# Kernel tuning notes

Measured on AMD Instinct MI355X. Metric: run time of the kernel, lower is better.

Reference implementation:

```python
import jax, jax.numpy as jnp
import numpy as np


def _conv2d(x, w, b, padding):
    # x: [N,C,H,W], w: [O,I,kh,kw]
    y = jax.lax.conv_general_dilated(
        x, w, window_strides=(1, 1), padding=padding,
        dimension_numbers=("NCHW", "OIHW", "NCHW"))
    return y + b[None, :, None, None]


def setup_inputs() -> dict:
    key = jax.random.key(0)
    ks = jax.random.split(key, 9)
    s = 0.05
    return {
        "x": jax.random.normal(ks[0], (16, 4, 512, 512), dtype=jnp.float32),
        "w1": jax.random.normal(ks[1], (32, 4, 3, 3), dtype=jnp.float32) * s,
        "b1": jax.random.normal(ks[2], (32,), dtype=jnp.float32) * s,
        "w2": jax.random.normal(ks[3], (4, 32, 3, 3), dtype=jnp.float32) * s,
        "b2": jax.random.normal(ks[4], (4,), dtype=jnp.float32) * s,
        "w_se1": jax.random.normal(ks[5], (16, 32, 1, 1), dtype=jnp.float32) * s,
        "b_se1": jax.random.normal(ks[6], (16,), dtype=jnp.float32) * s,
        "w_se2": jax.random.normal(ks[7], (32, 16, 1, 1), dtype=jnp.float32) * s,
        "b_se2": jax.random.normal(ks[8], (32,), dtype=jnp.float32) * s,
    }


def reference(x, w1, b1, w2, b2, w_se1, b_se1, w_se2, b_se2):
    x1 = x
    # module1: 3x3 conv (4->32) + ReLU
    h = jax.nn.relu(_conv2d(x, w1, b1, padding="SAME"))  # [N,32,H,W]
    se_in = h
    # SE branch: global avg pool -> 1x1 conv -> ReLU -> 1x1 conv -> sigmoid
    p = jnp.mean(h, axis=(2, 3), keepdims=True)  # [N,32,1,1]
    p = jax.nn.relu(_conv2d(p, w_se1, b_se1, padding="VALID"))  # [N,16,1,1]
    p = jax.nn.sigmoid(_conv2d(p, w_se2, b_se2, padding="VALID"))  # [N,32,1,1]
    h = p * se_in  # broadcast channel scaling
    # module2: 3x3 conv (32->4) + ReLU
    h = jax.nn.relu(_conv2d(h, w2, b2, padding="SAME"))  # [N,4,H,W]
    return h * x1  # residual multiply
```

## Files before the change

kernel.cpp:

```cpp
#include <hip/hip_runtime.h>
#include <math.h>

#define IMG 512

typedef __attribute__((ext_vector_type(4))) short short4_t;
typedef __attribute__((ext_vector_type(8))) short short8;
typedef __attribute__((ext_vector_type(4))) float f32x4;
typedef __attribute__((ext_vector_type(16))) float f32x16;
typedef __attribute__((ext_vector_type(2))) unsigned int u32x2;

__device__ __forceinline__ unsigned short f2bf(float f) {
  unsigned u = __builtin_bit_cast(unsigned, f);
  u += 0x7FFFu + ((u >> 16) & 1u);
  return (unsigned short)(u >> 16);
}
__device__ __forceinline__ unsigned cvtpk(float lo, float hi) {
  unsigned r;
  asm("v_cvt_pk_bf16_f32 %0, %1, %2" : "=v"(r) : "v"(lo), "v"(hi));
  return r;
}

__global__ __launch_bounds__(256) void k_prep(const float* __restrict__ w1,
                                              unsigned short* __restrict__ w1f) {
  const int t = threadIdx.x;
  if (t < 192) {
    const int kk = t >> 6, lane = t & 63;
    const int oc = lane & 31, hi = lane >> 5;
#pragma unroll
    for (int j = 0; j < 8; ++j) {
      const int dxp = 2 * hi + (j >> 2), ic = j & 3;
      float v = (dxp < 3) ? w1[((oc * 4 + ic) * 3 + kk) * 3 + dxp] : 0.f;
      w1f[(kk * 64 + lane) * 8 + j] = f2bf(v);
    }
  }
}

__global__ __launch_bounds__(256, 3) void k_pool(
    const float* __restrict__ x, const unsigned short* __restrict__ w1f,
    const float* __restrict__ b1, float* __restrict__ red_out, int use_atomic) {
  __shared__ unsigned short xs[34 * 40 * 4];
  __shared__ float pools[4][2][16];
  const int bid = blockIdx.x;
  const int swz = (bid & 7) * 512 + (bid >> 3);
  const int bx = swz & 15, by = (swz >> 4) & 15, n = swz >> 8;
  const int x0 = bx * 32, y0 = by * 32;
  const int t = threadIdx.x, lane = t & 63, wv = t >> 6;
  const int hi = lane >> 5;

  short8 A1[3];
#pragma unroll
  for (int kk = 0; kk < 3; ++kk)
    A1[kk] = *(const short8*)&w1f[(kk * 64 + lane) * 8];
  float bias_r[16];
#pragma unroll
  for (int r = 0; r < 16; ++r) {
    float bl = b1[(r & 3) + 8 * (r >> 2)], bh = b1[(r & 3) + 8 * (r >> 2) + 4];
    bias_r[r] = hi ? bh : bl;
  }

  const int sx = x0 - 4;
  const long CS = (long)IMG * IMG;
  for (int i = t; i < 340; i += 256) {
    const int row = i / 10, cb = i % 10;
    const int gy = y0 - 1 + row, gx0 = sx + cb * 4;
    f32x4 v0 = {0.f, 0.f, 0.f, 0.f}, v1 = v0, v2 = v0, v3 = v0;
    if (gy >= 0 && gy < IMG && gx0 >= 0 && gx0 < IMG) {
      const float* p = x + (((long)(n * 4) * IMG + gy) * IMG + gx0);
      v0 = *(const f32x4*)p;
      v1 = *(const f32x4*)(p + CS);
      v2 = *(const f32x4*)(p + 2 * CS);
      v3 = *(const f32x4*)(p + 3 * CS);
    }
    unsigned short* d = &xs[(row * 40 + cb * 4) * 4];
#pragma unroll
    for (int j = 0; j < 4; ++j) {
      u32x2 w;
      w[0] = cvtpk(v0[j], v1[j]);
      w[1] = cvtpk(v2[j], v3[j]);
      *(u32x2*)(d + j * 4) = w;
    }
  }
  __syncthreads();

  float pacc[16];
#pragma unroll
  for (int r = 0; r < 16; ++r) pacc[r] = 0.f;
  const int cx0 = (lane & 31) + 2 * hi + 3;
  const unsigned short* pP = &xs[((wv * 8) * 40 + cx0) * 4];
#define LOADP(K)                                                              \
  __builtin_shufflevector(*(const short4_t*)(pP + (K)*160),                   \
                          *(const short4_t*)(pP + (K)*160 + 4), 0, 1, 2, 3,   \
                          4, 5, 6, 7)
  short8 Ba, Bb, Bc;
  Ba = LOADP(0);
  Bb = LOADP(1);
#define P_ITER(IT, B0, B1, B2)                                                \
  {                                                                           \
    B2 = LOADP((IT) + 2);                                                     \
    f32x16 C;                                                                 \
    _Pragma("unroll") for (int r = 0; r < 16; ++r) C[r] = bias_r[r];          \
    C = __builtin_amdgcn_mfma_f32_32x32x16_bf16(A1[0], B0, C, 0, 0, 0);       \
    C = __builtin_amdgcn_mfma_f32_32x32x16_bf16(A1[1], B1, C, 0, 0, 0);       \
    C = __builtin_amdgcn_mfma_f32_32x32x16_bf16(A1[2], B2, C, 0, 0, 0);       \
    _Pragma("unroll") for (int r = 0; r < 16; ++r)                            \
        pacc[r] += fmaxf(C[r], 0.f);                                          \
  }
  P_ITER(0, Ba, Bb, Bc)
  P_ITER(1, Bb, Bc, Ba)
  P_ITER(2, Bc, Ba, Bb)
  P_ITER(3, Ba, Bb, Bc)
  P_ITER(4, Bb, Bc, Ba)
  P_ITER(5, Bc, Ba, Bb)
  P_ITER(6, Ba, Bb, Bc)
  P_ITER(7, Bb, Bc, Ba)
#undef P_ITER
#undef LOADP
#pragma unroll
  for (int r = 0; r < 16; ++r) {
#pragma unroll
    for (int m = 1; m < 32; m <<= 1) pacc[r] += __shfl_xor(pacc[r], m);
  }
  if ((lane & 31) == 0) {
#pragma unroll
    for (int r = 0; r < 16; ++r) pools[wv][hi][r] = pacc[r];
  }
  __syncthreads();
  if (t < 32) {
    const int c = t;
    const int hic = (c >> 2) & 1, reg = (c & 3) + 4 * (c >> 3);
    float s = pools[0][hic][reg] + pools[1][hic][reg] + pools[2][hic][reg] +
              pools[3][hic][reg];
    if (use_atomic) {
      atomicAdd(&red_out[n * 32 + c], s);
    } else {
      red_out[(n * 256 + by * 16 + bx) * 32 + c] = s;
    }
  }
}

__global__ __launch_bounds__(256) void k_se(
    const float* __restrict__ partials, const float* __restrict__ sums,
    const float* __restrict__ w_se1, const float* __restrict__ b_se1,
    const float* __restrict__ w_se2, const float* __restrict__ b_se2,
    const float* __restrict__ w2, unsigned short* __restrict__ w2f, int det) {
  const int n = blockIdx.x, t = threadIdx.x;
  __shared__ float red[8][32];
  __shared__ float mean_s[32], f1[16], p[32];
  if (det) {
    const int c = t & 31, s = t >> 5;
    float a = 0.f;
    for (int i = s * 32; i < s * 32 + 32; ++i)
      a += partials[(n * 256 + i) * 32 + c];
    red[s][c] = a;
    __syncthreads();
    if (t < 32) {
      float v = 0.f;
#pragma unroll
      for (int s2 = 0; s2 < 8; ++s2) v += red[s2][t];
      mean_s[t] = v * (1.0f / (512.f * 512.f));
    }
  } else {
    if (t < 32) mean_s[t] = sums[n * 32 + t] * (1.0f / (512.f * 512.f));
  }
  __syncthreads();
  if (t < 16) {
    float a = b_se1[t];
#pragma unroll
    for (int c = 0; c < 32; ++c) a += w_se1[t * 32 + c] * mean_s[c];
    f1[t] = fmaxf(a, 0.f);
  }
  __syncthreads();
  if (t < 32) {
    float a = b_se2[t];
#pragma unroll
    for (int c = 0; c < 16; ++c) a += w_se2[t * 16 + c] * f1[c];
    p[t] = 1.f / (1.f + expf(-a));
  }
  __syncthreads();
  for (int i = t; i < 9216; i += 256) {
    const int s = i >> 9, rem = i & 511, lane2 = rem >> 3, j = rem & 7;
    const int oc = lane2 & 3, yo = (lane2 >> 2) & 3, cg = lane2 >> 4;
    const int c = cg * 8 + j;
    const int dyy = s / 3, dx = s - dyy * 3, dy = dyy - yo;
    float v = 0.f;
    if (dy >= 0 && dy < 3) v = w2[(oc * 32 + c) * 9 + dy * 3 + dx] * p[c];
    w2f[((n * 18 + s) * 64 + lane2) * 8 + j] = f2bf(v);
  }
}

__global__ __launch_bounds__(256, 5) void k_main(
    const float* __restrict__ x, const unsigned short* __restrict__ w1f,
    const float* __restrict__ b1, const unsigned short* __restrict__ w2f,
    const float* __restrict__ b2, float* __restrict__ out) {
  __shared__ unsigned short xs[12 * 40 * 4];
  __shared__ unsigned short hs[10 * 32 * 32];
  const int bid = blockIdx.x;
  const int swz = (bid & 7) * 2304 + (bid >> 3);
  const int bx = swz % 18;
  const int q = swz / 18;
  const int by = q & 63, n = q >> 6;
  const int x0 = bx * 30, ytile = by * 8;
  const int t = threadIdx.x, lane = t & 63, wv = t >> 6;
  const int hi = lane >> 5;
  const long CS = (long)IMG * IMG;

  short8 A1[3];
#pragma unroll
  for (int kk = 0; kk < 3; ++kk)
    A1[kk] = *(const short8*)&w1f[(kk * 64 + lane) * 8];
  float bias_r[16];
#pragma unroll
  for (int r = 0; r < 16; ++r) {
    float bl = b1[(r & 3) + 8 * (r >> 2)], bh = b1[(r & 3) + 8 * (r >> 2) + 4];
    bias_r[r] = hi ? bh : bl;
  }

  const int sx = (x0 - 4) & ~3;
  if (t < 120) {
    const int row = t / 10, cb = t % 10;
    const int gy = ytile - 2 + row, gx0 = sx + cb * 4;
    f32x4 v0 = {0.f, 0.f, 0.f, 0.f}, v1 = v0, v2 = v0, v3 = v0;
    if (gy >= 0 && gy < IMG && gx0 >= 0 && gx0 < IMG) {
      const float* p = x + (((long)(n * 4) * IMG + gy) * IMG + gx0);
      v0 = *(const f32x4*)p;
      v1 = *(const f32x4*)(p + CS);
      v2 = *(const f32x4*)(p + 2 * CS);
      v3 = *(const f32x4*)(p + 3 * CS);
    }
    unsigned short* d = &xs[(row * 40 + cb * 4) * 4];
#pragma unroll
    for (int j = 0; j < 4; ++j) {
      u32x2 w;
      w[0] = cvtpk(v0[j], v1[j]);
      w[1] = cvtpk(v2[j], v3[j]);
      *(u32x2*)(d + j * 4) = w;
    }
  }
  __syncthreads();

  {
    const int px = lane & 31;
    const int cx0 = px + 2 * hi + (x0 - 2 - sx);
    const int q2 = (px >> 1) & 3;
    const int gxc = x0 - 1 + px;
    const bool colok = (gxc >= 0) && (gxc < IMG);
    const bool col_int = (x0 >= 1) && (x0 + 30 < IMG);
    const int R0 = (wv < 2) ? 3 * wv : 6 + 2 * (wv - 2);
    const unsigned short* pR = &xs[(R0 * 40 + cx0) * 4];
#define LOADX(K)                                                              \
  __builtin_shufflevector(*(const short4_t*)(pR + (K)*160),                   \
                          *(const short4_t*)(pR + (K)*160 + 4), 0, 1, 2, 3,   \
                          4, 5, 6, 7)
    short8 Ba, Bb, Bc;
    Ba = LOADX(0);
    Bb = LOADX(1);
#define C1_ITER(IT, B0, B1, B2)                                               \
  {                                                                           \
    B2 = LOADX((IT) + 2);                                                     \
    const int hy = R0 + (IT);                                                 \
    const int yi = ytile - 1 + hy;                                            \
    const bool row_ok = (yi >= 0) && (yi < IMG);                              \
    f32x16 C;                                                                 \
    _Pragma("unroll") for (int r = 0; r < 16; ++r) C[r] = bias_r[r];          \
    C = __builtin_amdgcn_mfma_f32_32x32x16_bf16(A1[0], B0, C, 0, 0, 0);       \
    C = __builtin_amdgcn_mfma_f32_32x32x16_bf16(A1[1], B1, C, 0, 0, 0);       \
    C = __builtin_amdgcn_mfma_f32_32x32x16_bf16(A1[2], B2, C, 0, 0, 0);       \
    const int usb = hy * 1024 + px * 32 + (hi << 2);                          \
    if (row_ok && col_int) {                                                  \
      _Pragma("unroll") for (int g = 0; g < 4; ++g) {                         \
        u32x2 w;                                                              \
        w[0] = cvtpk(fmaxf(C[4 * g + 0], 0.f), fmaxf(C[4 * g + 1], 0.f));     \
        w[1] = cvtpk(fmaxf(C[4 * g + 2], 0.f), fmaxf(C[4 * g + 3], 0.f));     \
        *(u32x2*)&hs[usb + ((g ^ q2) << 3)] = w;                              \
      }                                                                       \
    } else if (row_ok) {                                                      \
      _Pragma("unroll") for (int g = 0; g < 4; ++g) {                         \
        unsigned p01 =                                                        \
            cvtpk(fmaxf(C[4 * g + 0], 0.f), fmaxf(C[4 * g + 1], 0.f));        \
        unsigned p23 =                                                        \
            cvtpk(fmaxf(C[4 * g + 2], 0.f), fmaxf(C[4 * g + 3], 0.f));        \
        u32x2 w;                                                              \
        w[0] = colok ? p01 : 0u;                                              \
        w[1] = colok ? p23 : 0u;                                              \
        *(u32x2*)&hs[usb + ((g ^ q2) << 3)] = w;                              \
      }                                                                       \
    } else {                                                                  \
      u32x2 z;                                                                \
      z[0] = 0u;                                                              \
      z[1] = 0u;                                                              \
      _Pragma("unroll") for (int g = 0; g < 4; ++g)                           \
          *(u32x2*)&hs[usb + ((g ^ q2) << 3)] = z;                            \
    }                                                                         \
  }
    C1_ITER(0, Ba, Bb, Bc)
    C1_ITER(1, Bb, Bc, Ba)
    if (wv < 2) C1_ITER(2, Bc, Ba, Bb)
#undef C1_ITER
#undef LOADX
  }
  __syncthreads();

  {
    const int px16 = lane & 15, cg = lane >> 4;
    const int grp = wv & 1, wrow = wv >> 1;
    const int ox = grp * 16 + px16;
    const int yo = lane >> 4;
    const int gxo = x0 + ox;
    const bool epi_ok = (ox < 30) && (gxo < IMG);
    const float b20 = b2[0], b21 = b2[1], b22 = b2[2], b23 = b2[3];
    int ph0 = ox, ph1 = ox + 1, ph2 = ox + 2;
    ph2 = ph2 < 31 ? ph2 : 31;
    ph1 = ph1 < 31 ? ph1 : 31;
    const int ba0 = ph0 * 64 + ((cg ^ ((ph0 >> 1) & 3)) << 4);
    const int ba1 = ph1 * 64 + ((cg ^ ((ph1 >> 1) & 3)) << 4);
    const int ba2 = ph2 * 64 + ((cg ^ ((ph2 >> 1) & 3)) << 4);
    const char* hb = (const char*)hs + (wrow * 4) * 2048;
    const unsigned short* w2b = w2f + (size_t)n * 9216 + lane * 8;
    f32x4 CA = {b20, b21, b22, b23};
    short8 F0, F1, F2;

#define A2F(S) (*(const short8*)(w2b + (S)*512))
#define LOADF(R)                                                              \
  F0 = *(const short8*)(hb + (R)*2048 + ba0);                                 \
  F1 = *(const short8*)(hb + (R)*2048 + ba1);                                 \
  F2 = *(const short8*)(hb + (R)*2048 + ba2);
#define MFA(S0, S1, S2)                                                       \
  CA = __builtin_amdgcn_mfma_f32_16x16x32_bf16(A2F(S0), F0, CA, 0, 0, 0);     \
  CA = __builtin_amdgcn_mfma_f32_16x16x32_bf16(A2F(S1), F1, CA, 0, 0, 0);     \
  CA = __builtin_amdgcn_mfma_f32_16x16x32_bf16(A2F(S2), F2, CA, 0, 0, 0);

    __builtin_amdgcn_s_setprio(1);
    LOADF(0) MFA(0, 1, 2)
    LOADF(1) MFA(3, 4, 5)
    LOADF(2) MFA(6, 7, 8)
    LOADF(3) MFA(9, 10, 11)
    LOADF(4) MFA(12, 13, 14)
    LOADF(5) MFA(15, 16, 17)
    __builtin_amdgcn_s_setprio(0);
#undef LOADF
#undef MFA
#undef A2F

    if (epi_ok) {
      const int gy = ytile + wrow * 4 + yo;
      const long i0 = ((long)(n * 4) * IMG + gy) * IMG + gxo;
      out[i0] = fmaxf(CA[0], 0.f) * x[i0];
      out[i0 + CS] = fmaxf(CA[1], 0.f) * x[i0 + CS];
      out[i0 + 2 * CS] = fmaxf(CA[2], 0.f) * x[i0 + 2 * CS];
      out[i0 + 3 * CS] = fmaxf(CA[3], 0.f) * x[i0 + 3 * CS];
    }
  }
}

extern "C" void kernel_launch(void* const* d_in, const int* in_sizes, int n_in,
                              void* d_out, int out_size, void* d_ws,
                              size_t ws_size, hipStream_t stream) {
  const float* x = (const float*)d_in[0];
  const float* w1 = (const float*)d_in[1];
  const float* b1 = (const float*)d_in[2];
  const float* w2 = (const float*)d_in[3];
  const float* b2 = (const float*)d_in[4];
  const float* w_se1 = (const float*)d_in[5];
  const float* b_se1 = (const float*)d_in[6];
  const float* w_se2 = (const float*)d_in[7];
  const float* b_se2 = (const float*)d_in[8];
  float* out = (float*)d_out;
  float* ws = (float*)d_ws;

  float* sums = ws;
  unsigned short* w1f = (unsigned short*)(ws + 512);
  unsigned short* w2f = w1f + 1536;
  float* partials = (float*)(w2f + 147456);
  const size_t need_full =
      512 * 4 + 1536 * 2 + (size_t)147456 * 2 + (size_t)131072 * 4;

  k_prep<<<1, 256, 0, stream>>>(w1, w1f);
  if (ws_size >= need_full) {
    k_pool<<<4096, 256, 0, stream>>>(x, w1f, b1, partials, 0);
    k_se<<<16, 256, 0, stream>>>(partials, sums, w_se1, b_se1, w_se2, b_se2,
                                 w2, w2f, 1);
  } else {
    hipMemsetAsync(sums, 0, 512 * sizeof(float), stream);
    k_pool<<<4096, 256, 0, stream>>>(x, w1f, b1, sums, 1);
    k_se<<<16, 256, 0, stream>>>(partials, sums, w_se1, b_se1, w_se2, b_se2,
                                 w2, w2f, 0);
  }
  k_main<<<18432, 256, 0, stream>>>(x, w1f, b1, w2f, b2, out);
}
```

Before: 113.1 us.

## Process two row phases per block and reuse staged input for residual

```diff
diff --git a/kernel.cpp b/kernel.cpp
--- a/kernel.cpp
+++ b/kernel.cpp
@@ -18,6 +18,9 @@
   unsigned r;
   asm("v_cvt_pk_bf16_f32 %0, %1, %2" : "=v"(r) : "v"(lo), "v"(hi));
   return r;
+}
+__device__ __forceinline__ float bf2f(unsigned short v) {
+  return __builtin_bit_cast(float, ((unsigned)v) << 16);
 }
 
 __global__ __launch_bounds__(256) void k_prep(const float* __restrict__ w1,
@@ -188,21 +191,20 @@
   }
 }
 
-__global__ __launch_bounds__(256, 5) void k_main(
+__global__ __launch_bounds__(256, 4) void k_main(
     const float* __restrict__ x, const unsigned short* __restrict__ w1f,
     const float* __restrict__ b1, const unsigned short* __restrict__ w2f,
     const float* __restrict__ b2, float* __restrict__ out) {
-  __shared__ unsigned short xs[12 * 40 * 4];
+  __shared__ unsigned short xs[20 * 40 * 4];
   __shared__ unsigned short hs[10 * 32 * 32];
   const int bid = blockIdx.x;
-  const int swz = (bid & 7) * 2304 + (bid >> 3);
+  const int swz = (bid & 7) * 1152 + (bid >> 3);
   const int bx = swz % 18;
   const int q = swz / 18;
-  const int by = q & 63, n = q >> 6;
-  const int x0 = bx * 30, ytile = by * 8;
+  const int by = q & 31, n = q >> 5;
+  const int x0 = bx * 30, y0 = by * 16;
   const int t = threadIdx.x, lane = t & 63, wv = t >> 6;
   const int hi = lane >> 5;
-  const long CS = (long)IMG * IMG;
 
   short8 A1[3];
 #pragma unroll
@@ -216,9 +218,10 @@
   }
 
   const int sx = (x0 - 4) & ~3;
-  if (t < 120) {
-    const int row = t / 10, cb = t % 10;
-    const int gy = ytile - 2 + row, gx0 = sx + cb * 4;
+  const long CS = (long)IMG * IMG;
+  for (int i = t; i < 200; i += 256) {
+    const int row = i / 10, cb = i % 10;
+    const int gy = y0 - 2 + row, gx0 = sx + cb * 4;
     f32x4 v0 = {0.f, 0.f, 0.f, 0.f}, v1 = v0, v2 = v0, v3 = v0;
     if (gy >= 0 && gy < IMG && gx0 >= 0 && gx0 < IMG) {
       const float* p = x + (((long)(n * 4) * IMG + gy) * IMG + gx0);
@@ -238,27 +241,41 @@
   }
   __syncthreads();
 
-  {
-    const int px = lane & 31;
-    const int cx0 = px + 2 * hi + (x0 - 2 - sx);
-    const int q2 = (px >> 1) & 3;
-    const int gxc = x0 - 1 + px;
-    const bool colok = (gxc >= 0) && (gxc < IMG);
-    const bool col_int = (x0 >= 1) && (x0 + 30 < IMG);
-    const int R0 = (wv < 2) ? 3 * wv : 6 + 2 * (wv - 2);
-    const unsigned short* pR = &xs[(R0 * 40 + cx0) * 4];
+  const int px = lane & 31;
+  const int cx0 = px + 2 * hi + (x0 - 2 - sx);
+  const int q2 = (px >> 1) & 3;
+  const int gxc = x0 - 1 + px;
+  const bool colok = (gxc >= 0) && (gxc < IMG);
+  const bool col_int = (x0 >= 1) && (x0 + 30 < IMG);
+  const int R0 = (wv < 2) ? 3 * wv : 6 + 2 * (wv - 2);
+
+  const int px16 = lane & 15, cg = lane >> 4;
+  const int grp = wv & 1, ybq = wv >> 1;
+  const int ox = grp * 16 + px16;
+  const int yo = lane >> 4;
+  const int gxo = x0 + ox;
+  const bool epi_ok = (ox < 30) && (gxo < IMG);
+  const float b20 = b2[0], b21 = b2[1], b22 = b2[2], b23 = b2[3];
+  const int n4 = n * 4;
+  int ph0 = ox, ph1 = ox + 1, ph2 = ox + 2;
+  ph2 = ph2 < 31 ? ph2 : 31;
+  ph1 = ph1 < 31 ? ph1 : 31;
+  const int ba0 = ph0 * 64 + ((cg ^ ((ph0 >> 1) & 3)) << 4);
+  const int ba1 = ph1 * 64 + ((cg ^ ((ph1 >> 1) & 3)) << 4);
+  const int ba2 = ph2 * 64 + ((cg ^ ((ph2 >> 1) & 3)) << 4);
+  const char* hb = (const char*)hs + (ybq * 4) * 2048;
+  const int xcol = ox + (x0 - sx);
+  const unsigned short* w2b = w2f + (size_t)n * 9216 + lane * 8;
+
 #define LOADX(K)                                                              \
   __builtin_shufflevector(*(const short4_t*)(pR + (K)*160),                   \
                           *(const short4_t*)(pR + (K)*160 + 4), 0, 1, 2, 3,   \
                           4, 5, 6, 7)
-    short8 Ba, Bb, Bc;
-    Ba = LOADX(0);
-    Bb = LOADX(1);
-#define C1_ITER(IT, B0, B1, B2)                                               \
+#define C1_ITER(P, IT, B0, B1, B2)                                            \
   {                                                                           \
     B2 = LOADX((IT) + 2);                                                     \
     const int hy = R0 + (IT);                                                 \
-    const int yi = ytile - 1 + hy;                                            \
+    const int yi = y0 - 1 + (P)*8 + hy;                                       \
     const bool row_ok = (yi >= 0) && (yi < IMG);                              \
     f32x16 C;                                                                 \
     _Pragma("unroll") for (int r = 0; r < 16; ++r) C[r] = bias_r[r];          \
@@ -292,64 +309,84 @@
           *(u32x2*)&hs[usb + ((g ^ q2) << 3)] = z;                            \
     }                                                                         \
   }
-    C1_ITER(0, Ba, Bb, Bc)
-    C1_ITER(1, Bb, Bc, Ba)
-    if (wv < 2) C1_ITER(2, Bc, Ba, Bb)
-#undef C1_ITER
-#undef LOADX
-  }
-  __syncthreads();
-
-  {
-    const int px16 = lane & 15, cg = lane >> 4;
-    const int grp = wv & 1, wrow = wv >> 1;
-    const int ox = grp * 16 + px16;
-    const int yo = lane >> 4;
-    const int gxo = x0 + ox;
-    const bool epi_ok = (ox < 30) && (gxo < IMG);
-    const float b20 = b2[0], b21 = b2[1], b22 = b2[2], b23 = b2[3];
-    int ph0 = ox, ph1 = ox + 1, ph2 = ox + 2;
-    ph2 = ph2 < 31 ? ph2 : 31;
-    ph1 = ph1 < 31 ? ph1 : 31;
-    const int ba0 = ph0 * 64 + ((cg ^ ((ph0 >> 1) & 3)) << 4);
-    const int ba1 = ph1 * 64 + ((cg ^ ((ph1 >> 1) & 3)) << 4);
-    const int ba2 = ph2 * 64 + ((cg ^ ((ph2 >> 1) & 3)) << 4);
-    const char* hb = (const char*)hs + (wrow * 4) * 2048;
-    const unsigned short* w2b = w2f + (size_t)n * 9216 + lane * 8;
-    f32x4 CA = {b20, b21, b22, b23};
-    short8 F0, F1, F2;
-
-#define A2F(S) (*(const short8*)(w2b + (S)*512))
+#define CONV1_PHASE(P)                                                        \
+  {                                                                           \
+    const unsigned short* pR = &xs[(((P)*8 + R0) * 40 + cx0) * 4];            \
+    short8 Ba, Bb, Bc;                                                        \
+    Ba = LOADX(0);                                                            \
+    Bb = LOADX(1);                                                            \
+    C1_ITER(P, 0, Ba, Bb, Bc)                                                 \
+    C1_ITER(P, 1, Bb, Bc, Ba)                                                 \
+    if (wv < 2) C1_ITER(P, 2, Bc, Ba, Bb)                                     \
+  }
+
 #define LOADF(R)                                                              \
   F0 = *(const short8*)(hb + (R)*2048 + ba0);                                 \
   F1 = *(const short8*)(hb + (R)*2048 + ba1);                                 \
   F2 = *(const short8*)(hb + (R)*2048 + ba2);
 #define MFA(S0, S1, S2)                                                       \
-  CA = __builtin_amdgcn_mfma_f32_16x16x32_bf16(A2F(S0), F0, CA, 0, 0, 0);     \
-  CA = __builtin_amdgcn_mfma_f32_16x16x32_bf16(A2F(S1), F1, CA, 0, 0, 0);     \
-  CA = __builtin_amdgcn_mfma_f32_16x16x32_bf16(A2F(S2), F2, CA, 0, 0, 0);
-
-    __builtin_amdgcn_s_setprio(1);
-    LOADF(0) MFA(0, 1, 2)
-    LOADF(1) MFA(3, 4, 5)
-    LOADF(2) MFA(6, 7, 8)
-    LOADF(3) MFA(9, 10, 11)
-    LOADF(4) MFA(12, 13, 14)
-    LOADF(5) MFA(15, 16, 17)
-    __builtin_amdgcn_s_setprio(0);
+  CA = __builtin_amdgcn_mfma_f32_16x16x32_bf16(A2_##S0, F0, CA, 0, 0, 0);     \
+  CA = __builtin_amdgcn_mfma_f32_16x16x32_bf16(A2_##S1, F1, CA, 0, 0, 0);     \
+  CA = __builtin_amdgcn_mfma_f32_16x16x32_bf16(A2_##S2, F2, CA, 0, 0, 0);
+#define CONV2_PHASE(P)                                                        \
+  {                                                                           \
+    short8 A2_0 = *(const short8*)(w2b + 0 * 512);                            \
+    short8 A2_1 = *(const short8*)(w2b + 1 * 512);                            \
+    short8 A2_2 = *(const short8*)(w2b + 2 * 512);                            \
+    short8 A2_3 = *(const short8*)(w2b + 3 * 512);                            \
+    short8 A2_4 = *(const short8*)(w2b + 4 * 512);                            \
+    short8 A2_5 = *(const short8*)(w2b + 5 * 512);                            \
+    short8 A2_6 = *(const short8*)(w2b + 6 * 512);                            \
+    short8 A2_7 = *(const short8*)(w2b + 7 * 512);                            \
+    short8 A2_8 = *(const short8*)(w2b + 8 * 512);                            \
+    short8 A2_9 = *(const short8*)(w2b + 9 * 512);                            \
+    short8 A2_10 = *(const short8*)(w2b + 10 * 512);                          \
+    short8 A2_11 = *(const short8*)(w2b + 11 * 512);                          \
+    short8 A2_12 = *(const short8*)(w2b + 12 * 512);                          \
+    short8 A2_13 = *(const short8*)(w2b + 13 * 512);                          \
+    short8 A2_14 = *(const short8*)(w2b + 14 * 512);                          \
+    short8 A2_15 = *(const short8*)(w2b + 15 * 512);                          \
+    short8 A2_16 = *(const short8*)(w2b + 16 * 512);                          \
+    short8 A2_17 = *(const short8*)(w2b + 17 * 512);                          \
+    asm volatile("" ::"v"(A2_0), "v"(A2_1), "v"(A2_2), "v"(A2_3), "v"(A2_4),  \
+                 "v"(A2_5), "v"(A2_6), "v"(A2_7), "v"(A2_8), "v"(A2_9),       \
+                 "v"(A2_10), "v"(A2_11), "v"(A2_12), "v"(A2_13), "v"(A2_14),  \
+                 "v"(A2_15), "v"(A2_16), "v"(A2_17));                         \
+    __syncthreads();                                                          \
+    f32x4 CA = {b20, b21, b22, b23};                                          \
+    short8 F0, F1, F2;                                                        \
+    __builtin_amdgcn_s_setprio(1);                                            \
+    LOADF(0) MFA(0, 1, 2)                                                     \
+    LOADF(1) MFA(3, 4, 5)                                                     \
+    LOADF(2) MFA(6, 7, 8)                                                     \
+    LOADF(3) MFA(9, 10, 11)                                                   \
+    LOADF(4) MFA(12, 13, 14)                                                  \
+    LOADF(5) MFA(15, 16, 17)                                                  \
+    __builtin_amdgcn_s_setprio(0);                                            \
+    if (epi_ok) {                                                             \
+      const int gy = y0 + (P)*8 + ybq * 4 + yo;                               \
+      const long i0 = ((long)n4 * IMG + gy) * IMG + gxo;                      \
+      short4_t xv =                                                           \
+          *(const short4_t*)&xs[(((P)*8 + ybq * 4 + yo + 2) * 40 + xcol) * 4];\
+      out[i0] = fmaxf(CA[0], 0.f) * bf2f((unsigned short)xv[0]);              \
+      out[i0 + CS] = fmaxf(CA[1], 0.f) * bf2f((unsigned short)xv[1]);         \
+      out[i0 + 2 * CS] = fmaxf(CA[2], 0.f) * bf2f((unsigned short)xv[2]);     \
+      out[i0 + 3 * CS] = fmaxf(CA[3], 0.f) * bf2f((unsigned short)xv[3]);     \
+    }                                                                         \
+  }
+
+  CONV1_PHASE(0)
+  CONV2_PHASE(0)
+  __syncthreads();
+  CONV1_PHASE(1)
+  CONV2_PHASE(1)
+
+#undef CONV2_PHASE
+#undef MFA
 #undef LOADF
-#undef MFA
-#undef A2F
-
-    if (epi_ok) {
-      const int gy = ytile + wrow * 4 + yo;
-      const long i0 = ((long)(n * 4) * IMG + gy) * IMG + gxo;
-      out[i0] = fmaxf(CA[0], 0.f) * x[i0];
-      out[i0 + CS] = fmaxf(CA[1], 0.f) * x[i0 + CS];
-      out[i0 + 2 * CS] = fmaxf(CA[2], 0.f) * x[i0 + 2 * CS];
-      out[i0 + 3 * CS] = fmaxf(CA[3], 0.f) * x[i0 + 3 * CS];
-    }
-  }
+#undef CONV1_PHASE
+#undef C1_ITER
+#undef LOADX
 }
 
 extern "C" void kernel_launch(void* const* d_in, const int* in_sizes, int n_in,
@@ -385,5 +422,5 @@
     k_se<<<16, 256, 0, stream>>>(partials, sums, w_se1, b_se1, w_se2, b_se2,
                                  w2, w2f, 0);
   }
-  k_main<<<18432, 256, 0, stream>>>(x, w1f, b1, w2f, b2, out);
-}
+  k_main<<<9216, 256, 0, stream>>>(x, w1f, b1, w2f, b2, out);
+}
```

New measurement: 149.7 us. 1.32x slower.
